# Kernel optimization log

Hardware: AMD Instinct MI355X
Metric: run time of the kernel (lower is better)

Reference implementation:

```python
import jax, jax.numpy as jnp
import numpy as np

B, T, E, H = 2, 2048, 1024, 16
D = E // H  # head_size

def setup_inputs() -> dict:
    key = jax.random.key(0)
    ks = jax.random.split(key, 6)
    s = 0.02
    return {
        "x":  jax.random.normal(ks[0], (B, T, E), dtype=jnp.float32),
        "Wq": jax.random.normal(ks[1], (E, E), dtype=jnp.float32) * s,
        "Wk": jax.random.normal(ks[2], (E, E), dtype=jnp.float32) * s,
        "Wv": jax.random.normal(ks[3], (E, E), dtype=jnp.float32) * s,
        "Wp": jax.random.normal(ks[4], (E, E), dtype=jnp.float32) * s,
        "bp": jnp.zeros((E,), dtype=jnp.float32),
    }

def reference(x, Wq, Wk, Wv, Wp, bp):
    b, t, e = x.shape
    # Per-head Linear(E, D, bias=False) stacked == single [E,E] matmul then head split.
    # torch Linear: y = x @ W.T
    q = (x @ Wq.T).reshape(b, t, H, D).transpose(0, 2, 1, 3)  # (B,H,T,D)
    k = (x @ Wk.T).reshape(b, t, H, D).transpose(0, 2, 1, 3)
    v = (x @ Wv.T).reshape(b, t, H, D).transpose(0, 2, 1, 3)
    scale = jnp.asarray(D, x.dtype) ** -0.5
    wei = jnp.einsum('bhqd,bhkd->bhqk', q, k) * scale  # (B,H,T,T)
    causal = jnp.tril(jnp.ones((t, t), dtype=bool))
    wei = jnp.where(causal, wei, -jnp.inf)
    wei = jax.nn.softmax(wei, axis=-1)
    # dropout p=0.0 -> identity (eval-mode determinism)
    out = jnp.einsum('bhqk,bhkd->bhqd', wei, v)  # (B,H,T,D)
    out = out.transpose(0, 2, 1, 3).reshape(b, t, e)  # concat heads
    return out @ Wp.T + bp
```

## Files before the change

kernel.cpp:

```cpp
#include <hip/hip_runtime.h>

#define T_ 2048
#define E_ 1024
#define H_ 16
#define D_ 64
#define M_ 4096

typedef unsigned short ushort_t;
typedef __attribute__((ext_vector_type(8))) short bf16x8;
typedef __attribute__((ext_vector_type(4))) float f32x4;
typedef __attribute__((ext_vector_type(4))) unsigned short u16x4;
typedef __attribute__((ext_vector_type(8))) unsigned short u16x8;
typedef __attribute__((ext_vector_type(2))) unsigned int u32x2;

__device__ __forceinline__ ushort_t f2bf(float f) {
  union { float f; unsigned u; } v; v.f = f;
  unsigned r = v.u + 0x7FFFu + ((v.u >> 16) & 1u);
  return (ushort_t)(r >> 16);
}

__device__ __forceinline__ void gl16(const void* g, void* l) {
  __builtin_amdgcn_global_load_lds((const __attribute__((address_space(1))) void*)g,
                                   (__attribute__((address_space(3))) void*)l, 16, 0, 0);
}

__global__ __launch_bounds__(256)
void conv_all(const float* __restrict__ x,  const float* __restrict__ wq,
              const float* __restrict__ wk, const float* __restrict__ wv,
              const float* __restrict__ wp,
              ushort_t* __restrict__ xb,  ushort_t* __restrict__ wqb,
              ushort_t* __restrict__ wkb, ushort_t* __restrict__ wvb,
              ushort_t* __restrict__ wpb)
{
  const int id = blockIdx.x;
  const float* s; ushort_t* d; size_t off;
  if (id < 2048) { s = x; d = xb; off = (size_t)id * 2048; }
  else {
    int wsel = (id - 2048) >> 9, wid = (id - 2048) & 511;
    off = (size_t)wid * 2048;
    s = wsel == 0 ? wq : wsel == 1 ? wk : wsel == 2 ? wv : wp;
    d = wsel == 0 ? wqb : wsel == 1 ? wkb : wsel == 2 ? wvb : wpb;
  }
  size_t i = off + (size_t)threadIdx.x * 8;
  float4 a = *(const float4*)(s + i);
  float4 b = *(const float4*)(s + i + 4);
  u16x8 o;
  o[0]=f2bf(a.x); o[1]=f2bf(a.y); o[2]=f2bf(a.z); o[3]=f2bf(a.w);
  o[4]=f2bf(b.x); o[5]=f2bf(b.y); o[6]=f2bf(b.z); o[7]=f2bf(b.w);
  *(u16x8*)(d + i) = o;
}

__device__ __forceinline__ void gemm_core(const ushort_t* __restrict__ A,
                                          const ushort_t* __restrict__ W,
                                          int m0, int n0,
                                          ushort_t* As, ushort_t* Bs,
                                          f32x4 acc[4][4])
{
  const int t = threadIdx.x;
  const int lane = t & 63, w = t >> 6;
  const int g = lane >> 4, lq = lane & 15;
  const int wr = w >> 1, wc = w & 1;
  const int r0 = t >> 2;
  const int c0 = t & 3;
  const int ca0 = c0 ^ ((r0 >> 1) & 3);
  const int r1 = r0 + 64;
  const int ca1 = c0 ^ ((r1 >> 1) & 3);

  #pragma unroll
  for (int i = 0; i < 4; ++i)
    #pragma unroll
    for (int j = 0; j < 4; ++j) acc[i][j] = (f32x4){0.f,0.f,0.f,0.f};

  gl16(A + (size_t)(m0 + r0) * 1024 + ca0 * 8, As + t * 8);
  gl16(A + (size_t)(m0 + r1) * 1024 + ca1 * 8, As + 2048 + t * 8);
  gl16(W + (size_t)(n0 + r0) * 1024 + ca0 * 8, Bs + t * 8);
  gl16(W + (size_t)(n0 + r1) * 1024 + ca1 * 8, Bs + 2048 + t * 8);
  __syncthreads();

  int cur = 0;
  for (int k0 = 0; k0 < 1024; k0 += 32) {
    if (k0 + 32 < 1024) {
      const int nx = (cur ^ 1) * 4096;
      gl16(A + (size_t)(m0 + r0) * 1024 + k0 + 32 + ca0 * 8, As + nx + t * 8);
      gl16(A + (size_t)(m0 + r1) * 1024 + k0 + 32 + ca1 * 8, As + nx + 2048 + t * 8);
      gl16(W + (size_t)(n0 + r0) * 1024 + k0 + 32 + ca0 * 8, Bs + nx + t * 8);
      gl16(W + (size_t)(n0 + r1) * 1024 + k0 + 32 + ca1 * 8, Bs + nx + 2048 + t * 8);
    }
    const ushort_t* as = As + cur * 4096;
    const ushort_t* bs = Bs + cur * 4096;

    bf16x8 af[4], bfr[4];
    #pragma unroll
    for (int mi = 0; mi < 4; ++mi) {
      int row = wr * 64 + mi * 16 + lq;
      int ch = g ^ ((row >> 1) & 3);
      af[mi] = *(const bf16x8*)(as + row * 32 + ch * 8);
    }
    #pragma unroll
    for (int ni = 0; ni < 4; ++ni) {
      int row = wc * 64 + ni * 16 + lq;
      int ch = g ^ ((row >> 1) & 3);
      bfr[ni] = *(const bf16x8*)(bs + row * 32 + ch * 8);
    }
    __builtin_amdgcn_s_setprio(1);
    #pragma unroll
    for (int mi = 0; mi < 4; ++mi)
      #pragma unroll
      for (int ni = 0; ni < 4; ++ni)
        acc[mi][ni] = __builtin_amdgcn_mfma_f32_16x16x32_bf16(af[mi], bfr[ni], acc[mi][ni], 0, 0, 0);
    __builtin_amdgcn_s_setprio(0);

    __syncthreads();
    cur ^= 1;
  }
}

__global__ __launch_bounds__(256)
void gemm_qkv(const ushort_t* __restrict__ xb,
              const ushort_t* __restrict__ wqb, const ushort_t* __restrict__ wkb,
              const ushort_t* __restrict__ wvb,
              ushort_t* __restrict__ Qd, ushort_t* __restrict__ Kd, ushort_t* __restrict__ Vd)
{
  __shared__ __align__(16) ushort_t As[2 * 4096];
  __shared__ __align__(16) ushort_t Bs[2 * 4096];
  const int bx = blockIdx.x;
  const int sel = bx >> 3;
  const int n0 = (bx & 7) * 128;
  const int m0 = blockIdx.y * 128;
  const ushort_t* W = sel == 0 ? wqb : (sel == 1 ? wkb : wvb);
  f32x4 acc[4][4];
  gemm_core(xb, W, m0, n0, As, Bs, acc);

  const int t = threadIdx.x, lane = t & 63, w = t >> 6;
  const int g = lane >> 4, lq = lane & 15, wr = w >> 1, wc = w & 1;
  const float scl = (sel == 0) ? 0.125f : 1.0f;
  ushort_t* dst = sel == 0 ? Qd : (sel == 1 ? Kd : Vd);
  #pragma unroll
  for (int mi = 0; mi < 4; ++mi)
    #pragma unroll
    for (int ni = 0; ni < 4; ++ni)
      #pragma unroll
      for (int r = 0; r < 4; ++r) {
        int m = m0 + wr * 64 + mi * 16 + 4 * g + r;
        int n = n0 + wc * 64 + ni * 16 + lq;
        int b = m >> 11, tt = m & (T_ - 1);
        int h = n >> 6, d = n & (D_ - 1);
        ushort_t v = f2bf(acc[mi][ni][r] * scl);
        if (sel < 2) dst[((size_t)(b * H_ + h) * T_ + tt) * D_ + d] = v;
        else         dst[((size_t)(b * H_ + h) * D_ + d) * T_ + tt] = v;
      }
}

__global__ __launch_bounds__(256)
void gemm_out64(const ushort_t* __restrict__ Ab, const ushort_t* __restrict__ wpb,
                const float* __restrict__ bias, float* __restrict__ out)
{
  __shared__ __align__(16) ushort_t As[2 * 2048];
  __shared__ __align__(16) ushort_t Bs[2 * 4096];
  const int t = threadIdx.x, lane = t & 63, w = t >> 6;
  const int g = lane >> 4, lq = lane & 15;
  const int n0 = blockIdx.x * 128;
  const int m0 = blockIdx.y * 64;
  const int r0 = t >> 2, c0 = t & 3;
  const int ca0 = c0 ^ ((r0 >> 1) & 3);
  const int r1 = r0 + 64;
  const int ca1 = c0 ^ ((r1 >> 1) & 3);

  f32x4 acc[4][2];
  #pragma unroll
  for (int i = 0; i < 4; ++i) { acc[i][0] = (f32x4){0.f,0.f,0.f,0.f}; acc[i][1] = (f32x4){0.f,0.f,0.f,0.f}; }

  gl16(Ab  + (size_t)(m0 + r0) * 1024 + ca0 * 8, As + t * 8);
  gl16(wpb + (size_t)(n0 + r0) * 1024 + ca0 * 8, Bs + t * 8);
  gl16(wpb + (size_t)(n0 + r1) * 1024 + ca1 * 8, Bs + 2048 + t * 8);
  __syncthreads();

  int cur = 0;
  for (int k0 = 0; k0 < 1024; k0 += 32) {
    if (k0 + 32 < 1024) {
      gl16(Ab  + (size_t)(m0 + r0) * 1024 + k0 + 32 + ca0 * 8, As + (cur ^ 1) * 2048 + t * 8);
      gl16(wpb + (size_t)(n0 + r0) * 1024 + k0 + 32 + ca0 * 8, Bs + (cur ^ 1) * 4096 + t * 8);
      gl16(wpb + (size_t)(n0 + r1) * 1024 + k0 + 32 + ca1 * 8, Bs + (cur ^ 1) * 4096 + 2048 + t * 8);
    }
    const ushort_t* as = As + cur * 2048;
    const ushort_t* bs = Bs + cur * 4096;

    bf16x8 af[4], bfr[2];
    #pragma unroll
    for (int mi = 0; mi < 4; ++mi) {
      int row = mi * 16 + lq;
      int ch = g ^ ((row >> 1) & 3);
      af[mi] = *(const bf16x8*)(as + row * 32 + ch * 8);
    }
    #pragma unroll
    for (int ni = 0; ni < 2; ++ni) {
      int row = w * 32 + ni * 16 + lq;
      int ch = g ^ ((row >> 1) & 3);
      bfr[ni] = *(const bf16x8*)(bs + row * 32 + ch * 8);
    }
    __builtin_amdgcn_s_setprio(1);
    #pragma unroll
    for (int mi = 0; mi < 4; ++mi)
      #pragma unroll
      for (int ni = 0; ni < 2; ++ni)
        acc[mi][ni] = __builtin_amdgcn_mfma_f32_16x16x32_bf16(af[mi], bfr[ni], acc[mi][ni], 0, 0, 0);
    __builtin_amdgcn_s_setprio(0);

    __syncthreads();
    cur ^= 1;
  }
  #pragma unroll
  for (int mi = 0; mi < 4; ++mi)
    #pragma unroll
    for (int ni = 0; ni < 2; ++ni)
      #pragma unroll
      for (int r = 0; r < 4; ++r) {
        int m = m0 + mi * 16 + 4 * g + r;
        int n = n0 + w * 32 + ni * 16 + lq;
        out[(size_t)m * E_ + n] = acc[mi][ni][r] + bias[n];
      }
}

__global__ __launch_bounds__(256, 2)
void attn_mfma(const ushort_t* __restrict__ Q, const ushort_t* __restrict__ K,
               const ushort_t* __restrict__ Vt, ushort_t* __restrict__ O)
{
  __shared__ __align__(16) ushort_t Ps[128 * 72];
  const int t = threadIdx.x, w = t >> 6, lane = t & 63;
  const int g = lane >> 4, lq = lane & 15;
  const int i = blockIdx.x;
  const int xcd = i & 7, chunk = i >> 3;
  const int bh = xcd * 4 + (chunk >> 4);
  const int qt = (chunk < 32) ? (chunk & 15) : (15 - (chunk & 15));
  const int q0 = qt * 128;
  const size_t qkbase = (size_t)bh * T_ * D_;
  const size_t vbase  = (size_t)bh * D_ * T_;

  const int rowA = 32 * w + lq, rowB = rowA + 16;
  const int qgA = q0 + rowA, qgB = q0 + rowB;
  const bf16x8 qA0 = *(const bf16x8*)(Q + qkbase + (size_t)qgA * D_ + g * 8);
  const bf16x8 qA1 = *(const bf16x8*)(Q + qkbase + (size_t)qgA * D_ + 32 + g * 8);
  const bf16x8 qB0 = *(const bf16x8*)(Q + qkbase + (size_t)qgB * D_ + g * 8);
  const bf16x8 qB1 = *(const bf16x8*)(Q + qkbase + (size_t)qgB * D_ + 32 + g * 8);

  f32x4 accA[4], accB[4];
  #pragma unroll
  for (int db = 0; db < 4; ++db) { accA[db] = (f32x4){0.f,0.f,0.f,0.f}; accB[db] = (f32x4){0.f,0.f,0.f,0.f}; }
  float mA = -1e30f, lA = 0.f, mB = -1e30f, lB = 0.f;

  const int nt = 2 * qt + 2;

  for (int kt = 0; kt < nt; ++kt) {
    const int k0 = kt * 64;

    bf16x8 kf0[4], kf1[4], vf0[4], vf1[4];
    #pragma unroll
    for (int kb = 0; kb < 4; ++kb) {
      const ushort_t* kp = K + qkbase + (size_t)(k0 + kb * 16 + lq) * D_;
      kf0[kb] = *(const bf16x8*)(kp + g * 8);
      kf1[kb] = *(const bf16x8*)(kp + 32 + g * 8);
    }
    #pragma unroll
    for (int db = 0; db < 4; ++db) {
      const ushort_t* vp = Vt + vbase + (size_t)(db * 16 + lq) * T_ + k0;
      vf0[db] = *(const bf16x8*)(vp + g * 8);
      vf1[db] = *(const bf16x8*)(vp + 32 + g * 8);
    }

    f32x4 stA[4], stB[4];
    __builtin_amdgcn_s_setprio(1);
    #pragma unroll
    for (int kb = 0; kb < 4; ++kb) {
      f32x4 zA = (f32x4){0.f,0.f,0.f,0.f};
      zA = __builtin_amdgcn_mfma_f32_16x16x32_bf16(kf0[kb], qA0, zA, 0, 0, 0);
      zA = __builtin_amdgcn_mfma_f32_16x16x32_bf16(kf1[kb], qA1, zA, 0, 0, 0);
      stA[kb] = zA;
      f32x4 zB = (f32x4){0.f,0.f,0.f,0.f};
      zB = __builtin_amdgcn_mfma_f32_16x16x32_bf16(kf0[kb], qB0, zB, 0, 0, 0);
      zB = __builtin_amdgcn_mfma_f32_16x16x32_bf16(kf1[kb], qB1, zB, 0, 0, 0);
      stB[kb] = zB;
    }
    __builtin_amdgcn_s_setprio(0);

    if (kt >= nt - 2) {
      #pragma unroll
      for (int kb = 0; kb < 4; ++kb)
        #pragma unroll
        for (int r = 0; r < 4; ++r) {
          int kg = k0 + kb * 16 + 4 * g + r;
          if (kg > qgA) stA[kb][r] = -1e30f;
          if (kg > qgB) stB[kb][r] = -1e30f;
        }
    }

    float tmA = -1e30f, tmB = -1e30f;
    #pragma unroll
    for (int kb = 0; kb < 4; ++kb)
      #pragma unroll
      for (int r = 0; r < 4; ++r) { tmA = fmaxf(tmA, stA[kb][r]); tmB = fmaxf(tmB, stB[kb][r]); }
    tmA = fmaxf(tmA, __shfl_xor(tmA, 16)); tmA = fmaxf(tmA, __shfl_xor(tmA, 32));
    tmB = fmaxf(tmB, __shfl_xor(tmB, 16)); tmB = fmaxf(tmB, __shfl_xor(tmB, 32));

    if (!__all((tmA <= mA + 8.f) && (tmB <= mB + 8.f))) {
      float mnA = fmaxf(mA, tmA), mnB = fmaxf(mB, tmB);
      float alA = __expf(mA - mnA), alB = __expf(mB - mnB);
      mA = mnA; mB = mnB;
      lA *= alA; lB *= alB;
      float alAr[4], alBr[4];
      #pragma unroll
      for (int r = 0; r < 4; ++r) { alAr[r] = __shfl(alA, 4 * g + r); alBr[r] = __shfl(alB, 4 * g + r); }
      #pragma unroll
      for (int db = 0; db < 4; ++db)
        #pragma unroll
        for (int r = 0; r < 4; ++r) { accA[db][r] *= alAr[r]; accB[db][r] *= alBr[r]; }
    }

    float tsA = 0.f, tsB = 0.f;
    #pragma unroll
    for (int kb = 0; kb < 4; ++kb) {
      float pA0 = __expf(stA[kb][0] - mA), pA1 = __expf(stA[kb][1] - mA);
      float pA2 = __expf(stA[kb][2] - mA), pA3 = __expf(stA[kb][3] - mA);
      float pB0 = __expf(stB[kb][0] - mB), pB1 = __expf(stB[kb][1] - mB);
      float pB2 = __expf(stB[kb][2] - mB), pB3 = __expf(stB[kb][3] - mB);
      tsA += (pA0 + pA1) + (pA2 + pA3);
      tsB += (pB0 + pB1) + (pB2 + pB3);
      unsigned aLo, aHi, bLo, bHi;
      asm("v_cvt_pk_bf16_f32 %0, %1, %2" : "=v"(aLo) : "v"(pA0), "v"(pA1));
      asm("v_cvt_pk_bf16_f32 %0, %1, %2" : "=v"(aHi) : "v"(pA2), "v"(pA3));
      asm("v_cvt_pk_bf16_f32 %0, %1, %2" : "=v"(bLo) : "v"(pB0), "v"(pB1));
      asm("v_cvt_pk_bf16_f32 %0, %1, %2" : "=v"(bHi) : "v"(pB2), "v"(pB3));
      *(u32x2*)(Ps + rowA * 72 + kb * 16 + 4 * g) = (u32x2){aLo, aHi};
      *(u32x2*)(Ps + rowB * 72 + kb * 16 + 4 * g) = (u32x2){bLo, bHi};
    }
    tsA += __shfl_xor(tsA, 16); tsA += __shfl_xor(tsA, 32);
    tsB += __shfl_xor(tsB, 16); tsB += __shfl_xor(tsB, 32);
    lA += tsA; lB += tsB;

    asm volatile("s_waitcnt lgkmcnt(0)" ::: "memory");
    bf16x8 paA0 = *(const bf16x8*)(Ps + rowA * 72 + g * 8);
    bf16x8 paA1 = *(const bf16x8*)(Ps + rowA * 72 + 32 + g * 8);
    bf16x8 paB0 = *(const bf16x8*)(Ps + rowB * 72 + g * 8);
    bf16x8 paB1 = *(const bf16x8*)(Ps + rowB * 72 + 32 + g * 8);

    __builtin_amdgcn_s_setprio(1);
    #pragma unroll
    for (int db = 0; db < 4; ++db) {
      accA[db] = __builtin_amdgcn_mfma_f32_16x16x32_bf16(paA0, vf0[db], accA[db], 0, 0, 0);
      accA[db] = __builtin_amdgcn_mfma_f32_16x16x32_bf16(paA1, vf1[db], accA[db], 0, 0, 0);
      accB[db] = __builtin_amdgcn_mfma_f32_16x16x32_bf16(paB0, vf0[db], accB[db], 0, 0, 0);
      accB[db] = __builtin_amdgcn_mfma_f32_16x16x32_bf16(paB1, vf1[db], accB[db], 0, 0, 0);
    }
    __builtin_amdgcn_s_setprio(0);
  }

  float invA = 1.0f / lA, invB = 1.0f / lB;
  float liA[4], liB[4];
  #pragma unroll
  for (int r = 0; r < 4; ++r) { liA[r] = __shfl(invA, 4 * g + r); liB[r] = __shfl(invB, 4 * g + r); }
  const int b = bh >> 4, h = bh & 15;
  #pragma unroll
  for (int db = 0; db < 4; ++db)
    #pragma unroll
    for (int r = 0; r < 4; ++r) {
      int mAo = q0 + 32 * w + 4 * g + r;
      int mBo = mAo + 16;
      O[((size_t)(b * T_ + mAo)) * E_ + h * 64 + db * 16 + lq] = f2bf(accA[db][r] * liA[r]);
      O[((size_t)(b * T_ + mBo)) * E_ + h * 64 + db * 16 + lq] = f2bf(accB[db][r] * liB[r]);
    }
}

extern "C" void kernel_launch(void* const* d_in, const int* in_sizes, int n_in,
                              void* d_out, int out_size, void* d_ws, size_t ws_size,
                              hipStream_t stream) {
  const float* x  = (const float*)d_in[0];
  const float* Wq = (const float*)d_in[1];
  const float* Wk = (const float*)d_in[2];
  const float* Wv = (const float*)d_in[3];
  const float* Wp = (const float*)d_in[4];
  const float* bp = (const float*)d_in[5];
  float* out = (float*)d_out;

  ushort_t* ws  = (ushort_t*)d_ws;
  ushort_t* xb  = ws;
  ushort_t* wqb = xb  + (size_t)M_ * E_;
  ushort_t* wkb = wqb + (size_t)E_ * E_;
  ushort_t* wvb = wkb + (size_t)E_ * E_;
  ushort_t* wpb = wvb + (size_t)E_ * E_;
  ushort_t* Qb  = wpb + (size_t)E_ * E_;
  ushort_t* Kb  = Qb  + (size_t)M_ * E_;
  ushort_t* Vb  = Kb  + (size_t)M_ * E_;
  ushort_t* Ab  = Vb  + (size_t)M_ * E_;

  conv_all<<<4096, 256, 0, stream>>>(x, Wq, Wk, Wv, Wp, xb, wqb, wkb, wvb, wpb);
  gemm_qkv<<<dim3(24, 32), 256, 0, stream>>>(xb, wqb, wkb, wvb, Qb, Kb, Vb);
  attn_mfma<<<512, 256, 0, stream>>>(Qb, Kb, Vb, Ab);
  gemm_out64<<<dim3(8, 64), 256, 0, stream>>>(Ab, wpb, bp, out);
}
```

Measured before the change: 135.1 us.

## Stage K/V tiles through double-buffered swizzled LDS with async global-to-LDS loads

Each K and V tile is now loaded once per block into LDS with global_load_lds, double-buffered, using an XOR swizzle. Previously each of the four waves loaded the full K/V tile directly from global memory into registers. The change removes the 4x redundant global traffic and overlaps the prefetch of the next tile with compute on the current one. In exchange it adds 32KB of LDS, which may limit the 2-blocks-per-CU occupancy target, plus a barrier per iteration.

```diff
diff --git a/kernel.cpp b/kernel.cpp
--- a/kernel.cpp
+++ b/kernel.cpp
@@ -9,7 +9,6 @@
 typedef unsigned short ushort_t;
 typedef __attribute__((ext_vector_type(8))) short bf16x8;
 typedef __attribute__((ext_vector_type(4))) float f32x4;
-typedef __attribute__((ext_vector_type(4))) unsigned short u16x4;
 typedef __attribute__((ext_vector_type(8))) unsigned short u16x8;
 typedef __attribute__((ext_vector_type(2))) unsigned int u32x2;
 
@@ -225,6 +224,8 @@
 void attn_mfma(const ushort_t* __restrict__ Q, const ushort_t* __restrict__ K,
                const ushort_t* __restrict__ Vt, ushort_t* __restrict__ O)
 {
+  __shared__ __align__(16) ushort_t Ks[2][4096];
+  __shared__ __align__(16) ushort_t Vs[2][4096];
   __shared__ __align__(16) ushort_t Ps[128 * 72];
   const int t = threadIdx.x, w = t >> 6, lane = t & 63;
   const int g = lane >> 4, lq = lane & 15;
@@ -236,6 +237,10 @@
   const size_t qkbase = (size_t)bh * T_ * D_;
   const size_t vbase  = (size_t)bh * D_ * T_;
 
+  const int srow = t >> 3, sc = t & 7;
+  const int cs0 = sc ^ (srow & 7);
+  const int srow1 = srow + 32, cs1 = sc ^ (srow1 & 7);
+
   const int rowA = 32 * w + lq, rowB = rowA + 16;
   const int qgA = q0 + rowA, qgB = q0 + rowB;
   const bf16x8 qA0 = *(const bf16x8*)(Q + qkbase + (size_t)qgA * D_ + g * 8);
@@ -250,34 +255,40 @@
 
   const int nt = 2 * qt + 2;
 
+  gl16(K + qkbase + (size_t)srow  * D_ + cs0 * 8, &Ks[0][t * 8]);
+  gl16(K + qkbase + (size_t)srow1 * D_ + cs1 * 8, &Ks[0][2048 + t * 8]);
+  gl16(Vt + vbase + (size_t)srow  * T_ + cs0 * 8, &Vs[0][t * 8]);
+  gl16(Vt + vbase + (size_t)srow1 * T_ + cs1 * 8, &Vs[0][2048 + t * 8]);
+  asm volatile("s_waitcnt vmcnt(0)" ::: "memory");
+  __builtin_amdgcn_s_barrier();
+
   for (int kt = 0; kt < nt; ++kt) {
+    const int cur = kt & 1;
     const int k0 = kt * 64;
-
-    bf16x8 kf0[4], kf1[4], vf0[4], vf1[4];
-    #pragma unroll
-    for (int kb = 0; kb < 4; ++kb) {
-      const ushort_t* kp = K + qkbase + (size_t)(k0 + kb * 16 + lq) * D_;
-      kf0[kb] = *(const bf16x8*)(kp + g * 8);
-      kf1[kb] = *(const bf16x8*)(kp + 32 + g * 8);
-    }
-    #pragma unroll
-    for (int db = 0; db < 4; ++db) {
-      const ushort_t* vp = Vt + vbase + (size_t)(db * 16 + lq) * T_ + k0;
-      vf0[db] = *(const bf16x8*)(vp + g * 8);
-      vf1[db] = *(const bf16x8*)(vp + 32 + g * 8);
-    }
+    if (kt + 1 < nt) {
+      const int kn = (kt + 1) * 64;
+      gl16(K + qkbase + (size_t)(kn + srow)  * D_ + cs0 * 8, &Ks[cur ^ 1][t * 8]);
+      gl16(K + qkbase + (size_t)(kn + srow1) * D_ + cs1 * 8, &Ks[cur ^ 1][2048 + t * 8]);
+      gl16(Vt + vbase + (size_t)srow  * T_ + kn + cs0 * 8, &Vs[cur ^ 1][t * 8]);
+      gl16(Vt + vbase + (size_t)srow1 * T_ + kn + cs1 * 8, &Vs[cur ^ 1][2048 + t * 8]);
+    }
+    const ushort_t* kb_ = &Ks[cur][0];
+    const ushort_t* vb_ = &Vs[cur][0];
 
     f32x4 stA[4], stB[4];
     __builtin_amdgcn_s_setprio(1);
     #pragma unroll
     for (int kb = 0; kb < 4; ++kb) {
+      int krow = kb * 16 + lq;
+      bf16x8 ka0 = *(const bf16x8*)(kb_ + krow * 64 + ((g ^ (krow & 7)) * 8));
+      bf16x8 ka1 = *(const bf16x8*)(kb_ + krow * 64 + (((4 + g) ^ (krow & 7)) * 8));
       f32x4 zA = (f32x4){0.f,0.f,0.f,0.f};
-      zA = __builtin_amdgcn_mfma_f32_16x16x32_bf16(kf0[kb], qA0, zA, 0, 0, 0);
-      zA = __builtin_amdgcn_mfma_f32_16x16x32_bf16(kf1[kb], qA1, zA, 0, 0, 0);
+      zA = __builtin_amdgcn_mfma_f32_16x16x32_bf16(ka0, qA0, zA, 0, 0, 0);
+      zA = __builtin_amdgcn_mfma_f32_16x16x32_bf16(ka1, qA1, zA, 0, 0, 0);
       stA[kb] = zA;
       f32x4 zB = (f32x4){0.f,0.f,0.f,0.f};
-      zB = __builtin_amdgcn_mfma_f32_16x16x32_bf16(kf0[kb], qB0, zB, 0, 0, 0);
-      zB = __builtin_amdgcn_mfma_f32_16x16x32_bf16(kf1[kb], qB1, zB, 0, 0, 0);
+      zB = __builtin_amdgcn_mfma_f32_16x16x32_bf16(ka0, qB0, zB, 0, 0, 0);
+      zB = __builtin_amdgcn_mfma_f32_16x16x32_bf16(ka1, qB1, zB, 0, 0, 0);
       stB[kb] = zB;
     }
     __builtin_amdgcn_s_setprio(0);
@@ -345,12 +356,18 @@
     __builtin_amdgcn_s_setprio(1);
     #pragma unroll
     for (int db = 0; db < 4; ++db) {
-      accA[db] = __builtin_amdgcn_mfma_f32_16x16x32_bf16(paA0, vf0[db], accA[db], 0, 0, 0);
-      accA[db] = __builtin_amdgcn_mfma_f32_16x16x32_bf16(paA1, vf1[db], accA[db], 0, 0, 0);
-      accB[db] = __builtin_amdgcn_mfma_f32_16x16x32_bf16(paB0, vf0[db], accB[db], 0, 0, 0);
-      accB[db] = __builtin_amdgcn_mfma_f32_16x16x32_bf16(paB1, vf1[db], accB[db], 0, 0, 0);
+      int vrow = db * 16 + lq;
+      bf16x8 vb0 = *(const bf16x8*)(vb_ + vrow * 64 + ((g ^ (vrow & 7)) * 8));
+      bf16x8 vb1 = *(const bf16x8*)(vb_ + vrow * 64 + (((4 + g) ^ (vrow & 7)) * 8));
+      accA[db] = __builtin_amdgcn_mfma_f32_16x16x32_bf16(paA0, vb0, accA[db], 0, 0, 0);
+      accA[db] = __builtin_amdgcn_mfma_f32_16x16x32_bf16(paA1, vb1, accA[db], 0, 0, 0);
+      accB[db] = __builtin_amdgcn_mfma_f32_16x16x32_bf16(paB0, vb0, accB[db], 0, 0, 0);
+      accB[db] = __builtin_amdgcn_mfma_f32_16x16x32_bf16(paB1, vb1, accB[db], 0, 0, 0);
     }
     __builtin_amdgcn_s_setprio(0);
+
+    if (kt + 1 < nt) asm volatile("s_waitcnt vmcnt(0)" ::: "memory");
+    __builtin_amdgcn_s_barrier();
   }
 
   float invA = 1.0f / lA, invB = 1.0f / lB;
```

Measured after the change: 122.8 us. -9.1%, faster.

## Stage K/V tiles through double-buffered swizzled LDS with async global-to-LDS loads

Applied to the files above, without the earlier changes.

The attention kernel now loads K and V^T tiles with global_load_lds into XOR-swizzled, double-buffered shared memory, two 64-key tiles per stage. The next stage is prefetched while the current one is computed, replacing per-wave direct global loads that each wave issued redundantly. Block-to-(bh, q-tile) mapping changes to schedule heaviest q-tiles first, and the occupancy hint of 2 blocks per CU is dropped. The LDS footprint grows to about 82KB per block, which limits occupancy.

```diff
diff --git a/kernel.cpp b/kernel.cpp
--- a/kernel.cpp
+++ b/kernel.cpp
@@ -9,7 +9,6 @@
 typedef unsigned short ushort_t;
 typedef __attribute__((ext_vector_type(8))) short bf16x8;
 typedef __attribute__((ext_vector_type(4))) float f32x4;
-typedef __attribute__((ext_vector_type(4))) unsigned short u16x4;
 typedef __attribute__((ext_vector_type(8))) unsigned short u16x8;
 typedef __attribute__((ext_vector_type(2))) unsigned int u32x2;
 
@@ -221,20 +220,25 @@
       }
 }
 
-__global__ __launch_bounds__(256, 2)
+__global__ __launch_bounds__(256)
 void attn_mfma(const ushort_t* __restrict__ Q, const ushort_t* __restrict__ K,
                const ushort_t* __restrict__ Vt, ushort_t* __restrict__ O)
 {
+  __shared__ __align__(16) ushort_t Ks[2][8192];
+  __shared__ __align__(16) ushort_t Vs[2][8192];
   __shared__ __align__(16) ushort_t Ps[128 * 72];
   const int t = threadIdx.x, w = t >> 6, lane = t & 63;
   const int g = lane >> 4, lq = lane & 15;
   const int i = blockIdx.x;
-  const int xcd = i & 7, chunk = i >> 3;
-  const int bh = xcd * 4 + (chunk >> 4);
-  const int qt = (chunk < 32) ? (chunk & 15) : (15 - (chunk & 15));
+  const int qt = 15 - ((i & 255) >> 4);
+  const int bh = (i & 15) | ((i >> 8) << 4);
   const int q0 = qt * 128;
   const size_t qkbase = (size_t)bh * T_ * D_;
   const size_t vbase  = (size_t)bh * D_ * T_;
+
+  const int srow = t >> 3, sc = t & 7;
+  const int cs0 = sc ^ (srow & 7);
+  const int srow1 = srow + 32, cs1 = sc ^ (srow1 & 7);
 
   const int rowA = 32 * w + lq, rowB = rowA + 16;
   const int qgA = q0 + rowA, qgB = q0 + rowB;
@@ -249,109 +253,126 @@
   float mA = -1e30f, lA = 0.f, mB = -1e30f, lB = 0.f;
 
   const int nt = 2 * qt + 2;
-
-  for (int kt = 0; kt < nt; ++kt) {
-    const int k0 = kt * 64;
-
-    bf16x8 kf0[4], kf1[4], vf0[4], vf1[4];
-    #pragma unroll
-    for (int kb = 0; kb < 4; ++kb) {
-      const ushort_t* kp = K + qkbase + (size_t)(k0 + kb * 16 + lq) * D_;
-      kf0[kb] = *(const bf16x8*)(kp + g * 8);
-      kf1[kb] = *(const bf16x8*)(kp + 32 + g * 8);
-    }
-    #pragma unroll
-    for (int db = 0; db < 4; ++db) {
-      const ushort_t* vp = Vt + vbase + (size_t)(db * 16 + lq) * T_ + k0;
-      vf0[db] = *(const bf16x8*)(vp + g * 8);
-      vf1[db] = *(const bf16x8*)(vp + 32 + g * 8);
-    }
-
-    f32x4 stA[4], stB[4];
-    __builtin_amdgcn_s_setprio(1);
-    #pragma unroll
-    for (int kb = 0; kb < 4; ++kb) {
-      f32x4 zA = (f32x4){0.f,0.f,0.f,0.f};
-      zA = __builtin_amdgcn_mfma_f32_16x16x32_bf16(kf0[kb], qA0, zA, 0, 0, 0);
-      zA = __builtin_amdgcn_mfma_f32_16x16x32_bf16(kf1[kb], qA1, zA, 0, 0, 0);
-      stA[kb] = zA;
-      f32x4 zB = (f32x4){0.f,0.f,0.f,0.f};
-      zB = __builtin_amdgcn_mfma_f32_16x16x32_bf16(kf0[kb], qB0, zB, 0, 0, 0);
-      zB = __builtin_amdgcn_mfma_f32_16x16x32_bf16(kf1[kb], qB1, zB, 0, 0, 0);
-      stB[kb] = zB;
-    }
-    __builtin_amdgcn_s_setprio(0);
-
-    if (kt >= nt - 2) {
-      #pragma unroll
-      for (int kb = 0; kb < 4; ++kb)
-        #pragma unroll
-        for (int r = 0; r < 4; ++r) {
-          int kg = k0 + kb * 16 + 4 * g + r;
-          if (kg > qgA) stA[kb][r] = -1e30f;
-          if (kg > qgB) stB[kb][r] = -1e30f;
-        }
-    }
-
-    float tmA = -1e30f, tmB = -1e30f;
-    #pragma unroll
-    for (int kb = 0; kb < 4; ++kb)
-      #pragma unroll
-      for (int r = 0; r < 4; ++r) { tmA = fmaxf(tmA, stA[kb][r]); tmB = fmaxf(tmB, stB[kb][r]); }
-    tmA = fmaxf(tmA, __shfl_xor(tmA, 16)); tmA = fmaxf(tmA, __shfl_xor(tmA, 32));
-    tmB = fmaxf(tmB, __shfl_xor(tmB, 16)); tmB = fmaxf(tmB, __shfl_xor(tmB, 32));
-
-    if (!__all((tmA <= mA + 8.f) && (tmB <= mB + 8.f))) {
-      float mnA = fmaxf(mA, tmA), mnB = fmaxf(mB, tmB);
-      float alA = __expf(mA - mnA), alB = __expf(mB - mnB);
-      mA = mnA; mB = mnB;
-      lA *= alA; lB *= alB;
-      float alAr[4], alBr[4];
-      #pragma unroll
-      for (int r = 0; r < 4; ++r) { alAr[r] = __shfl(alA, 4 * g + r); alBr[r] = __shfl(alB, 4 * g + r); }
-      #pragma unroll
-      for (int db = 0; db < 4; ++db)
-        #pragma unroll
-        for (int r = 0; r < 4; ++r) { accA[db][r] *= alAr[r]; accB[db][r] *= alBr[r]; }
-    }
-
-    float tsA = 0.f, tsB = 0.f;
-    #pragma unroll
-    for (int kb = 0; kb < 4; ++kb) {
-      float pA0 = __expf(stA[kb][0] - mA), pA1 = __expf(stA[kb][1] - mA);
-      float pA2 = __expf(stA[kb][2] - mA), pA3 = __expf(stA[kb][3] - mA);
-      float pB0 = __expf(stB[kb][0] - mB), pB1 = __expf(stB[kb][1] - mB);
-      float pB2 = __expf(stB[kb][2] - mB), pB3 = __expf(stB[kb][3] - mB);
-      tsA += (pA0 + pA1) + (pA2 + pA3);
-      tsB += (pB0 + pB1) + (pB2 + pB3);
-      unsigned aLo, aHi, bLo, bHi;
-      asm("v_cvt_pk_bf16_f32 %0, %1, %2" : "=v"(aLo) : "v"(pA0), "v"(pA1));
-      asm("v_cvt_pk_bf16_f32 %0, %1, %2" : "=v"(aHi) : "v"(pA2), "v"(pA3));
-      asm("v_cvt_pk_bf16_f32 %0, %1, %2" : "=v"(bLo) : "v"(pB0), "v"(pB1));
-      asm("v_cvt_pk_bf16_f32 %0, %1, %2" : "=v"(bHi) : "v"(pB2), "v"(pB3));
-      *(u32x2*)(Ps + rowA * 72 + kb * 16 + 4 * g) = (u32x2){aLo, aHi};
-      *(u32x2*)(Ps + rowB * 72 + kb * 16 + 4 * g) = (u32x2){bLo, bHi};
-    }
-    tsA += __shfl_xor(tsA, 16); tsA += __shfl_xor(tsA, 32);
-    tsB += __shfl_xor(tsB, 16); tsB += __shfl_xor(tsB, 32);
-    lA += tsA; lB += tsB;
-
-    asm volatile("s_waitcnt lgkmcnt(0)" ::: "memory");
-    bf16x8 paA0 = *(const bf16x8*)(Ps + rowA * 72 + g * 8);
-    bf16x8 paA1 = *(const bf16x8*)(Ps + rowA * 72 + 32 + g * 8);
-    bf16x8 paB0 = *(const bf16x8*)(Ps + rowB * 72 + g * 8);
-    bf16x8 paB1 = *(const bf16x8*)(Ps + rowB * 72 + 32 + g * 8);
-
-    __builtin_amdgcn_s_setprio(1);
-    #pragma unroll
-    for (int db = 0; db < 4; ++db) {
-      accA[db] = __builtin_amdgcn_mfma_f32_16x16x32_bf16(paA0, vf0[db], accA[db], 0, 0, 0);
-      accA[db] = __builtin_amdgcn_mfma_f32_16x16x32_bf16(paA1, vf1[db], accA[db], 0, 0, 0);
-      accB[db] = __builtin_amdgcn_mfma_f32_16x16x32_bf16(paB0, vf0[db], accB[db], 0, 0, 0);
-      accB[db] = __builtin_amdgcn_mfma_f32_16x16x32_bf16(paB1, vf1[db], accB[db], 0, 0, 0);
-    }
-    __builtin_amdgcn_s_setprio(0);
+  const int nss = qt + 1;
+
+#define STAGE_TILE(K0_, KD_, VD_)                                              \
+  do {                                                                         \
+    gl16(K + qkbase + (size_t)((K0_) + srow)  * D_ + cs0 * 8, (KD_) + t * 8);  \
+    gl16(K + qkbase + (size_t)((K0_) + srow1) * D_ + cs1 * 8, (KD_) + 2048 + t * 8); \
+    gl16(Vt + vbase + (size_t)srow  * T_ + (K0_) + cs0 * 8, (VD_) + t * 8);    \
+    gl16(Vt + vbase + (size_t)srow1 * T_ + (K0_) + cs1 * 8, (VD_) + 2048 + t * 8);   \
+  } while (0)
+
+#define TILE_BODY(KT_, KB_, VB_)                                               \
+  do {                                                                         \
+    const int k0 = (KT_) * 64;                                                 \
+    const ushort_t* kb_ = (KB_);                                               \
+    const ushort_t* vb_ = (VB_);                                               \
+    f32x4 stA[4], stB[4];                                                      \
+    __builtin_amdgcn_s_setprio(1);                                             \
+    _Pragma("unroll")                                                          \
+    for (int kb = 0; kb < 4; ++kb) {                                           \
+      int krow = kb * 16 + lq;                                                 \
+      bf16x8 ka0 = *(const bf16x8*)(kb_ + krow * 64 + ((g ^ (krow & 7)) * 8)); \
+      bf16x8 ka1 = *(const bf16x8*)(kb_ + krow * 64 + (((4 + g) ^ (krow & 7)) * 8)); \
+      f32x4 zA = (f32x4){0.f,0.f,0.f,0.f};                                     \
+      zA = __builtin_amdgcn_mfma_f32_16x16x32_bf16(ka0, qA0, zA, 0, 0, 0);     \
+      zA = __builtin_amdgcn_mfma_f32_16x16x32_bf16(ka1, qA1, zA, 0, 0, 0);     \
+      stA[kb] = zA;                                                            \
+      f32x4 zB = (f32x4){0.f,0.f,0.f,0.f};                                     \
+      zB = __builtin_amdgcn_mfma_f32_16x16x32_bf16(ka0, qB0, zB, 0, 0, 0);     \
+      zB = __builtin_amdgcn_mfma_f32_16x16x32_bf16(ka1, qB1, zB, 0, 0, 0);     \
+      stB[kb] = zB;                                                            \
+    }                                                                          \
+    __builtin_amdgcn_s_setprio(0);                                             \
+    if ((KT_) >= nt - 2) {                                                     \
+      _Pragma("unroll")                                                        \
+      for (int kb = 0; kb < 4; ++kb)                                           \
+        _Pragma("unroll")                                                      \
+        for (int r = 0; r < 4; ++r) {                                          \
+          int kg = k0 + kb * 16 + 4 * g + r;                                   \
+          if (kg > qgA) stA[kb][r] = -1e30f;                                   \
+          if (kg > qgB) stB[kb][r] = -1e30f;                                   \
+        }                                                                      \
+    }                                                                          \
+    float tmA = -1e30f, tmB = -1e30f;                                          \
+    _Pragma("unroll")                                                          \
+    for (int kb = 0; kb < 4; ++kb)                                             \
+      _Pragma("unroll")                                                        \
+      for (int r = 0; r < 4; ++r) { tmA = fmaxf(tmA, stA[kb][r]); tmB = fmaxf(tmB, stB[kb][r]); } \
+    tmA = fmaxf(tmA, __shfl_xor(tmA, 16)); tmA = fmaxf(tmA, __shfl_xor(tmA, 32)); \
+    tmB = fmaxf(tmB, __shfl_xor(tmB, 16)); tmB = fmaxf(tmB, __shfl_xor(tmB, 32)); \
+    if (!__all((tmA <= mA + 8.f) && (tmB <= mB + 8.f))) {                      \
+      float mnA = fmaxf(mA, tmA), mnB = fmaxf(mB, tmB);                        \
+      float alA = __expf(mA - mnA), alB = __expf(mB - mnB);                    \
+      mA = mnA; mB = mnB;                                                      \
+      lA *= alA; lB *= alB;                                                    \
+      float alAr[4], alBr[4];                                                  \
+      _Pragma("unroll")                                                        \
+      for (int r = 0; r < 4; ++r) { alAr[r] = __shfl(alA, 4 * g + r); alBr[r] = __shfl(alB, 4 * g + r); } \
+      _Pragma("unroll")                                                        \
+      for (int db = 0; db < 4; ++db)                                           \
+        _Pragma("unroll")                                                      \
+        for (int r = 0; r < 4; ++r) { accA[db][r] *= alAr[r]; accB[db][r] *= alBr[r]; } \
+    }                                                                          \
+    float tsA = 0.f, tsB = 0.f;                                                \
+    _Pragma("unroll")                                                          \
+    for (int kb = 0; kb < 4; ++kb) {                                           \
+      float pA0 = __expf(stA[kb][0] - mA), pA1 = __expf(stA[kb][1] - mA);      \
+      float pA2 = __expf(stA[kb][2] - mA), pA3 = __expf(stA[kb][3] - mA);      \
+      float pB0 = __expf(stB[kb][0] - mB), pB1 = __expf(stB[kb][1] - mB);      \
+      float pB2 = __expf(stB[kb][2] - mB), pB3 = __expf(stB[kb][3] - mB);      \
+      tsA += (pA0 + pA1) + (pA2 + pA3);                                        \
+      tsB += (pB0 + pB1) + (pB2 + pB3);                                        \
+      unsigned aLo, aHi, bLo, bHi;                                             \
+      asm("v_cvt_pk_bf16_f32 %0, %1, %2" : "=v"(aLo) : "v"(pA0), "v"(pA1));    \
+      asm("v_cvt_pk_bf16_f32 %0, %1, %2" : "=v"(aHi) : "v"(pA2), "v"(pA3));    \
+      asm("v_cvt_pk_bf16_f32 %0, %1, %2" : "=v"(bLo) : "v"(pB0), "v"(pB1));    \
+      asm("v_cvt_pk_bf16_f32 %0, %1, %2" : "=v"(bHi) : "v"(pB2), "v"(pB3));    \
+      *(u32x2*)(Ps + rowA * 72 + kb * 16 + 4 * g) = (u32x2){aLo, aHi};         \
+      *(u32x2*)(Ps + rowB * 72 + kb * 16 + 4 * g) = (u32x2){bLo, bHi};         \
+    }                                                                          \
+    tsA += __shfl_xor(tsA, 16); tsA += __shfl_xor(tsA, 32);                    \
+    tsB += __shfl_xor(tsB, 16); tsB += __shfl_xor(tsB, 32);                    \
+    lA += tsA; lB += tsB;                                                      \
+    asm volatile("s_waitcnt lgkmcnt(0)" ::: "memory");                         \
+    bf16x8 paA0 = *(const bf16x8*)(Ps + rowA * 72 + g * 8);                    \
+    bf16x8 paA1 = *(const bf16x8*)(Ps + rowA * 72 + 32 + g * 8);               \
+    bf16x8 paB0 = *(const bf16x8*)(Ps + rowB * 72 + g * 8);                    \
+    bf16x8 paB1 = *(const bf16x8*)(Ps + rowB * 72 + 32 + g * 8);               \
+    __builtin_amdgcn_s_setprio(1);                                             \
+    _Pragma("unroll")                                                          \
+    for (int db = 0; db < 4; ++db) {                                           \
+      int vrow = db * 16 + lq;                                                 \
+      bf16x8 vb0 = *(const bf16x8*)(vb_ + vrow * 64 + ((g ^ (vrow & 7)) * 8)); \
+      bf16x8 vb1 = *(const bf16x8*)(vb_ + vrow * 64 + (((4 + g) ^ (vrow & 7)) * 8)); \
+      accA[db] = __builtin_amdgcn_mfma_f32_16x16x32_bf16(paA0, vb0, accA[db], 0, 0, 0); \
+      accA[db] = __builtin_amdgcn_mfma_f32_16x16x32_bf16(paA1, vb1, accA[db], 0, 0, 0); \
+      accB[db] = __builtin_amdgcn_mfma_f32_16x16x32_bf16(paB0, vb0, accB[db], 0, 0, 0); \
+      accB[db] = __builtin_amdgcn_mfma_f32_16x16x32_bf16(paB1, vb1, accB[db], 0, 0, 0); \
+    }                                                                          \
+    __builtin_amdgcn_s_setprio(0);                                             \
+  } while (0)
+
+  STAGE_TILE(0,  &Ks[0][0],    &Vs[0][0]);
+  STAGE_TILE(64, &Ks[0][4096], &Vs[0][4096]);
+  asm volatile("s_waitcnt vmcnt(0)" ::: "memory");
+  __builtin_amdgcn_s_barrier();
+
+  for (int ss = 0; ss < nss; ++ss) {
+    const int cur = ss & 1;
+    if (ss + 1 < nss) {
+      const int kn = (2 * ss + 2) * 64;
+      STAGE_TILE(kn,      &Ks[cur ^ 1][0],    &Vs[cur ^ 1][0]);
+      STAGE_TILE(kn + 64, &Ks[cur ^ 1][4096], &Vs[cur ^ 1][4096]);
+    }
+    TILE_BODY(2 * ss,     &Ks[cur][0],    &Vs[cur][0]);
+    TILE_BODY(2 * ss + 1, &Ks[cur][4096], &Vs[cur][4096]);
+    if (ss + 1 < nss) asm volatile("s_waitcnt vmcnt(0)" ::: "memory");
+    __builtin_amdgcn_s_barrier();
   }
+#undef STAGE_TILE
+#undef TILE_BODY
 
   float invA = 1.0f / lA, invB = 1.0f / lB;
   float liA[4], liB[4];
```

Measured after the change: 127.7 us. 5.5% less time.
